# Performance work log

Measured on AMD Instinct MI355X. Metric: run time of the kernel, lower is better.

## Reference

```python
import jax, jax.numpy as jnp
import numpy as np

HIDDEN = 1024
HEADS = 16
HEAD = HIDDEN // HEADS
EXPAND = 4096
EPS = 1e-5


def layer_norm(x, g, b):
    mu = jnp.mean(x, axis=-1, keepdims=True)
    var = jnp.mean((x - mu) ** 2, axis=-1, keepdims=True)
    return (x - mu) * jax.lax.rsqrt(var + EPS) * g + b


def setup_inputs() -> dict:
    key = jax.random.key(0)
    ks = jax.random.split(key, 12)
    s = 0.02
    return {
        "x": jax.random.normal(ks[0], (4, 2048, HIDDEN), dtype=jnp.float32),
        "Wqkv": jax.random.normal(ks[1], (HIDDEN, 3 * HIDDEN), dtype=jnp.float32) * s,
        "bqkv": jnp.zeros((3 * HIDDEN,), jnp.float32),
        "Wproj": jax.random.normal(ks[2], (HIDDEN, HIDDEN), dtype=jnp.float32) * s,
        "bproj": jnp.zeros((HIDDEN,), jnp.float32),
        "W1": jax.random.normal(ks[3], (HIDDEN, EXPAND), dtype=jnp.float32) * s,
        "b1": jnp.zeros((EXPAND,), jnp.float32),
        "W2": jax.random.normal(ks[4], (EXPAND, HIDDEN), dtype=jnp.float32) * s,
        "b2": jnp.zeros((HIDDEN,), jnp.float32),
        "g1": jnp.ones((HIDDEN,), jnp.float32),
        "be1": jnp.zeros((HIDDEN,), jnp.float32),
        "g2": jnp.ones((HIDDEN,), jnp.float32),
        "be2": jnp.zeros((HIDDEN,), jnp.float32),
    }


def attention(x, Wqkv, bqkv, Wproj, bproj):
    B, L, _ = x.shape
    qkv = (x @ Wqkv + bqkv).reshape(B, L, 3, HEADS, HEAD)
    q, k, v = [qkv[:, :, i].transpose(0, 2, 1, 3) for i in range(3)]  # [B,H,L,D]
    attn = jnp.einsum("bnld,bnkd->bnlk", q, k) / np.sqrt(HEAD).astype(np.float32)
    attn = jax.nn.softmax(attn, axis=-1)
    o = jnp.einsum("bnlk,bnkd->bnld", attn, v)
    o = o.transpose(0, 2, 1, 3).reshape(B, L, HIDDEN)
    return o @ Wproj + bproj


def reference(x, Wqkv, bqkv, Wproj, bproj, W1, b1, W2, b2, g1, be1, g2, be2):
    # post-norm transformer block (pre_norm=False), dropout=0 (eval)
    h = layer_norm(x + attention(x, Wqkv, bqkv, Wproj, bproj), g1, be1)
    ff = jax.nn.gelu(h @ W1 + b1, approximate=False) @ W2 + b2
    return layer_norm(h + ff, g2, be2)
```

## Files before the change

### kernel.cpp

```cpp
#include <hip/hip_runtime.h>
#include <hip/hip_bf16.h>
#include <math.h>


typedef __bf16 bf16_t;
typedef __bf16 bf16x8 __attribute__((ext_vector_type(8)));
typedef __bf16 bf16x4 __attribute__((ext_vector_type(4)));
typedef float f32x4 __attribute__((ext_vector_type(4)));
typedef float f32x16 __attribute__((ext_vector_type(16)));

#define HID   1024
#define NHEAD 16
#define HD    64
#define EXPD  4096
#define LSEQ  2048
#define BATCH 4
#define MROWS (BATCH * LSEQ)

#if __has_builtin(__builtin_amdgcn_exp2f)
#define EXP2F __builtin_amdgcn_exp2f
#else
#define EXP2F exp2f
#endif

__device__ __forceinline__ void gld_lds16(const bf16_t* g, bf16_t* l) {
  __builtin_amdgcn_global_load_lds(
      (const __attribute__((address_space(1))) void*)g,
      (__attribute__((address_space(3))) void*)l, 16, 0, 0);
}

__device__ __forceinline__ void vmwait(int n) {
  if (n == 8)      asm volatile("s_waitcnt vmcnt(8)" ::: "memory");
  else if (n == 4) asm volatile("s_waitcnt vmcnt(4)" ::: "memory");
  else if (n == 3) asm volatile("s_waitcnt vmcnt(3)" ::: "memory");
  else if (n == 0) asm volatile("s_waitcnt vmcnt(0)" ::: "memory");
}

__device__ __forceinline__ void block_bar() {
  asm volatile("" ::: "memory");
  __builtin_amdgcn_s_barrier();
  asm volatile("" ::: "memory");
}

__device__ __forceinline__ void swap32(unsigned& a, unsigned& b) {
#if __has_builtin(__builtin_amdgcn_permlane32_swap)
  auto r = __builtin_amdgcn_permlane32_swap(a, b, false, false);
  a = r[0]; b = r[1];
#else
  bool hiL = ((threadIdx.x & 63) >= 32);
  unsigned pa = (unsigned)__shfl_xor((int)a, 32, 64);
  unsigned pb = (unsigned)__shfl_xor((int)b, 32, 64);
  unsigned na = hiL ? pb : a;
  unsigned nb = hiL ? b : pa;
  a = na; b = nb;
#endif
}

__device__ __forceinline__ unsigned pk_bf16(float lo, float hi) {
  bf16_t l = (bf16_t)lo, h = (bf16_t)hi;
  unsigned short ul, uh;
  __builtin_memcpy(&ul, &l, 2);
  __builtin_memcpy(&uh, &h, 2);
  return (unsigned)ul | ((unsigned)uh << 16);
}

__global__ __launch_bounds__(256) void cvt_bf16(const float* __restrict__ in,
                                                bf16_t* __restrict__ out, int n4) {
  int i = blockIdx.x * 256 + threadIdx.x;
  if (i >= n4) return;
  float4 v = ((const float4*)in)[i];
  bf16x4 o;
  o[0] = (bf16_t)v.x; o[1] = (bf16_t)v.y; o[2] = (bf16_t)v.z; o[3] = (bf16_t)v.w;
  ((bf16x4*)out)[i] = o;
}

__global__ __launch_bounds__(256) void transpose_cvt(const float* __restrict__ W,
                                                     bf16_t* __restrict__ Wt,
                                                     int K, int N) {
  __shared__ float tile[32][33];
  int n0 = blockIdx.x * 32, k0 = blockIdx.y * 32;
  int tx = threadIdx.x & 31, ty = threadIdx.x >> 5;
#pragma unroll
  for (int i = 0; i < 32; i += 8)
    tile[ty + i][tx] = W[(size_t)(k0 + ty + i) * N + n0 + tx];
  __syncthreads();
#pragma unroll
  for (int i = 0; i < 32; i += 8)
    Wt[(size_t)(n0 + ty + i) * K + k0 + tx] = (bf16_t)tile[tx][ty + i];
}

__global__ __launch_bounds__(256) void transpose_v(const bf16_t* __restrict__ qkvb,
                                                   bf16_t* __restrict__ vT) {
  __shared__ bf16_t tile[64][65];
  const int l0 = blockIdx.x * 64;
  const int bh = blockIdx.y;
  const int b = bh >> 4, h = bh & 15;
  const int tx = threadIdx.x & 63, ty = threadIdx.x >> 6;
  const bf16_t* src = qkvb + ((size_t)(b * LSEQ + l0)) * 3072 + 2048 + h * 64;
#pragma unroll
  for (int i = 0; i < 16; ++i) {
    int l = ty + 4 * i;
    tile[l][tx] = src[(size_t)l * 3072 + tx];
  }
  __syncthreads();
  bf16_t* dst = vT + ((size_t)bh * HD) * LSEQ + l0;
#pragma unroll
  for (int i = 0; i < 16; ++i) {
    int d = ty + 4 * i;
    dst[(size_t)d * LSEQ + tx] = tile[tx][d];
  }
}

template <int BM, int BN, int NTHR>
__global__ __launch_bounds__(NTHR, (NTHR == 512 ? 4 : 3))
void gemm_k(const bf16_t* __restrict__ A,
            const bf16_t* __restrict__ Bt,
            const float* __restrict__ bias,
            void* __restrict__ C,
            int M, int N, int K, int mode) {
  constexpr int WC = (NTHR / 64) / 2;
  constexpr int AL = BM * 4 / NTHR;
  constexpr int BL = BN * 4 / NTHR;
  constexpr int LOADS = AL + BL;
  constexpr int RSTEP = NTHR >> 2;
  __shared__ bf16_t As[3 * BM * 32];
  __shared__ bf16_t Bs[3 * BN * 32];

  const int nbx = gridDim.x;
  int p = blockIdx.y * nbx + blockIdx.x;
  const int GM = 8;
  int group = p / (GM * nbx);
  int idx = p - group * (GM * nbx);
  const int by = group * GM + (idx & (GM - 1));
  const int bx = idx >> 3;
  const int n0 = bx * BN, m0 = by * BM;

  const int t = threadIdx.x;
  const int lane = t & 63, w = t >> 6;
  const int wr = w / WC, wc = w % WC;
  const int quad = lane >> 4, l16 = lane & 15;

  f32x4 acc[4][4];
#pragma unroll
  for (int i = 0; i < 4; ++i)
#pragma unroll
    for (int j = 0; j < 4; ++j) acc[i][j] = (f32x4){0.f, 0.f, 0.f, 0.f};

  const int r0 = t >> 2;
  const unsigned ksw = (((unsigned)t & 3u) ^ ((unsigned)(r0 >> 1) & 3u)) * 8u;
  const unsigned offR0 = (unsigned)r0 * (unsigned)K + ksw;

  const bf16_t* aB = A + (size_t)m0 * K;
  const bf16_t* bB = Bt + (size_t)n0 * K;

  unsigned aoff[4], boff[4];
#pragma unroll
  for (int i = 0; i < 4; ++i) {
    int row = wr * 64 + 16 * i + l16;
    aoff[i] = (unsigned)(row * 32 + (quad ^ ((row >> 1) & 3)) * 8);
  }
#pragma unroll
  for (int j = 0; j < 4; ++j) {
    int row = wc * 64 + 16 * j + l16;
    boff[j] = (unsigned)(row * 32 + (quad ^ ((row >> 1) & 3)) * 8);
  }

  auto stage = [&](int slot, int kk) {
    bf16_t* Asl = As + slot * (BM * 32);
    bf16_t* Bsl = Bs + slot * (BN * 32);
    const bf16_t* aS = aB + kk;
    const bf16_t* bS = bB + kk;
#pragma unroll
    for (int a = 0; a < AL; ++a)
      gld_lds16(aS + offR0 + (size_t)a * RSTEP * K, Asl + (t + a * NTHR) * 8);
#pragma unroll
    for (int b = 0; b < BL; ++b)
      gld_lds16(bS + offR0 + (size_t)b * RSTEP * K, Bsl + (t + b * NTHR) * 8);
  };

  const int NT = K >> 5;

  stage(0, 0);
  stage(1, 32);
  vmwait(LOADS);
  block_bar();

  int cs = 0;
  for (int kt = 0; kt < NT; ++kt) {
    if (kt < NT - 2) {
      int ss = cs == 0 ? 2 : cs - 1;
      stage(ss, (kt + 2) * 32);
    }
    const bf16_t* Asl = As + cs * (BM * 32);
    const bf16_t* Bsl = Bs + cs * (BN * 32);
    bf16x8 af[4], bfr[4];
#pragma unroll
    for (int i = 0; i < 4; ++i) af[i] = *(const bf16x8*)(Asl + aoff[i]);
#pragma unroll
    for (int j = 0; j < 4; ++j) bfr[j] = *(const bf16x8*)(Bsl + boff[j]);
    __builtin_amdgcn_s_setprio(1);
#pragma unroll
    for (int i = 0; i < 4; ++i)
#pragma unroll
      for (int j = 0; j < 4; ++j)
        acc[i][j] = __builtin_amdgcn_mfma_f32_16x16x32_bf16(af[i], bfr[j], acc[i][j], 0, 0, 0);
    __builtin_amdgcn_s_setprio(0);
    if (kt < NT - 2)      vmwait(LOADS);
    else if (kt == NT - 2) vmwait(0);
    if (kt < NT - 1) block_bar();
    cs = cs == 2 ? 0 : cs + 1;
  }

#pragma unroll
  for (int i = 0; i < 4; ++i) {
    int rowb = m0 + wr * 64 + 16 * i + quad * 4;
#pragma unroll
    for (int j = 0; j < 4; ++j) {
      int col = n0 + wc * 64 + 16 * j + l16;
      float bv = bias[col];
#pragma unroll
      for (int r = 0; r < 4; ++r) {
        float v = acc[i][j][r] + bv;
        size_t idx = (size_t)(rowb + r) * N + col;
        if (mode == 0) {
          ((bf16_t*)C)[idx] = (bf16_t)v;
        } else if (mode == 1) {
          float u = v * (0.7978845608028654f + 0.0356774081f * v * v);
          float e = EXP2F(u * 2.885390082f);
          float th = (e - 1.f) / (e + 1.f);
          float gel = 0.5f * v * (1.f + th);
          ((bf16_t*)C)[idx] = (bf16_t)gel;
        } else {
          ((float*)C)[idx] = v;
        }
      }
    }
  }
}

__global__ __launch_bounds__(256, 2) void attn_kernel(const bf16_t* __restrict__ qkv,
                                                      const bf16_t* __restrict__ vT,
                                                      bf16_t* __restrict__ ob) {
  __shared__ bf16_t smem[5 * 128 * 64];
  bf16_t* Qs = smem + 32768;
  const int qt = blockIdx.x, h = blockIdx.y, b = blockIdx.z;
  const int t = threadIdx.x, lane = t & 63, w = t >> 6;
  const int l32 = lane & 31, hi = lane >> 5;
  const size_t RS = 3 * HID;
  const int bh = b * NHEAD + h;

  const bf16_t* qbase = qkv + ((size_t)(b * LSEQ + qt * 128)) * RS + h * HD;
  const bf16_t* kbase = qkv + ((size_t)b * LSEQ) * RS + HID + h * HD;
  const bf16_t* vtbase = vT + (size_t)bh * HD * LSEQ;

#pragma unroll
  for (int s = 0; s < 4; ++s) {
    int l = t + s * 256;
    int r = l >> 3, c8 = l & 7;
    gld_lds16(qbase + (size_t)r * RS + ((c8 ^ (r & 7)) * 8), Qs + l * 8);
  }
  __syncthreads();

  const float sc = 0.18033688011112042f;
  bf16x8 bq[4];
  {
    int qrow = 32 * w + l32;
#pragma unroll
    for (int c = 0; c < 4; ++c) {
      int y = 2 * c + hi;
      bf16x8 q8 = *(const bf16x8*)(Qs + qrow * 64 + ((y ^ (qrow & 7)) * 8));
#pragma unroll
      for (int e = 0; e < 8; ++e) q8[e] = (bf16_t)((float)q8[e] * sc);
      bq[c] = q8;
    }
  }

  auto stageKV = [&](int slot, int kt) {
    bf16_t* Ks = smem + slot * 16384;
    bf16_t* Vts = Ks + 8192;
#pragma unroll
    for (int s = 0; s < 4; ++s) {
      int l = t + s * 256;
      int r = l >> 3, c8 = l & 7;
      gld_lds16(kbase + (size_t)(kt * 128 + r) * RS + ((c8 ^ (r & 7)) * 8), Ks + l * 8);
      int rv = l >> 4, c16 = l & 15;
      gld_lds16(vtbase + (size_t)rv * LSEQ + kt * 128 + ((c16 ^ (rv & 7)) * 8), Vts + l * 8);
    }
  };

  f32x16 accO[2];
#pragma unroll
  for (int dt = 0; dt < 2; ++dt)
#pragma unroll
    for (int e = 0; e < 16; ++e) accO[dt][e] = 0.f;
  float l_acc = 0.f;

  constexpr int NT = LSEQ / 128;
  stageKV(0, 0);

  for (int kt = 0; kt < NT; ++kt) {
    const int cs = kt & 1;
    if (kt + 1 < NT) {
      stageKV(1 - cs, kt + 1);
      vmwait(8);
    } else {
      vmwait(0);
    }
    block_bar();
    const bf16_t* Ks = smem + cs * 16384;
    const bf16_t* Vts = Ks + 8192;

#pragma unroll
    for (int kt2 = 0; kt2 < 2; ++kt2) {
      f32x16 s0, s1;
#pragma unroll
      for (int e = 0; e < 16; ++e) { s0[e] = 0.f; s1[e] = 0.f; }
      __builtin_amdgcn_s_setprio(1);
#pragma unroll
      for (int c = 0; c < 4; ++c) {
        int y = 2 * c + hi;
        int r0 = (2 * kt2 + 0) * 32 + l32;
        bf16x8 a0 = *(const bf16x8*)(Ks + r0 * 64 + ((y ^ (r0 & 7)) * 8));
        s0 = __builtin_amdgcn_mfma_f32_32x32x16_bf16(a0, bq[c], s0, 0, 0, 0);
        int r1 = (2 * kt2 + 1) * 32 + l32;
        bf16x8 a1 = *(const bf16x8*)(Ks + r1 * 64 + ((y ^ (r1 & 7)) * 8));
        s1 = __builtin_amdgcn_mfma_f32_32x32x16_bf16(a1, bq[c], s1, 0, 0, 0);
      }
      __builtin_amdgcn_s_setprio(0);

      unsigned pf[2][2][4];
#pragma unroll
      for (int tile = 0; tile < 2; ++tile) {
        f32x16& sv = tile ? s1 : s0;
        float p[16];
#pragma unroll
        for (int e = 0; e < 16; ++e) { p[e] = EXP2F(sv[e]); l_acc += p[e]; }
        unsigned lo[4], hi_[4];
#pragma unroll
        for (int g = 0; g < 4; ++g) {
          lo[g] = pk_bf16(p[4 * g + 0], p[4 * g + 1]);
          hi_[g] = pk_bf16(p[4 * g + 2], p[4 * g + 3]);
        }
#pragma unroll
        for (int c2 = 0; c2 < 2; ++c2) {
          unsigned aL = lo[2 * c2], bL = lo[2 * c2 + 1];
          swap32(aL, bL);
          pf[tile][c2][0] = aL; pf[tile][c2][2] = bL;
          unsigned aH = hi_[2 * c2], bH = hi_[2 * c2 + 1];
          swap32(aH, bH);
          pf[tile][c2][1] = aH; pf[tile][c2][3] = bH;
        }
      }

      __builtin_amdgcn_s_setprio(1);
#pragma unroll
      for (int dt = 0; dt < 2; ++dt)
#pragma unroll
        for (int tile = 0; tile < 2; ++tile)
#pragma unroll
          for (int c2 = 0; c2 < 2; ++c2) {
            int ktile = 2 * kt2 + tile;
            int c8v = ktile * 4 + c2 * 2 + hi;
            int rv = dt * 32 + l32;
            bf16x8 av = *(const bf16x8*)(Vts + rv * 128 + ((c8v ^ (rv & 7)) * 8));
            union { unsigned u[4]; bf16x8 v; } bp;
            bp.u[0] = pf[tile][c2][0]; bp.u[1] = pf[tile][c2][1];
            bp.u[2] = pf[tile][c2][2]; bp.u[3] = pf[tile][c2][3];
            accO[dt] = __builtin_amdgcn_mfma_f32_32x32x16_bf16(av, bp.v, accO[dt], 0, 0, 0);
          }
      __builtin_amdgcn_s_setprio(0);
    }
    block_bar();
  }

  l_acc += __shfl_xor(l_acc, 32, 64);
  float inv = 1.f / l_acc;

  bf16_t* Osh = smem;
  {
    int q = 32 * w + l32;
#pragma unroll
    for (int dt = 0; dt < 2; ++dt)
#pragma unroll
      for (int e = 0; e < 16; ++e) {
        int d = dt * 32 + (e & 3) + 8 * (e >> 2) + 4 * hi;
        Osh[q * 68 + d] = (bf16_t)(accO[dt][e] * inv);
      }
  }
  __syncthreads();
#pragma unroll
  for (int s = 0; s < 4; ++s) {
    int l = t + s * 256;
    int r = l >> 3, c8 = l & 7;
    bf16x8 v = *(const bf16x8*)(Osh + r * 68 + c8 * 8);
    *(bf16x8*)(ob + ((size_t)(b * LSEQ + qt * 128 + r)) * HID + h * HD + c8 * 8) = v;
  }
}

__global__ __launch_bounds__(256) void resid_ln(const float* __restrict__ X,
                                                const float* __restrict__ Y,
                                                const float* __restrict__ g,
                                                const float* __restrict__ be,
                                                float* __restrict__ outf,
                                                bf16_t* __restrict__ outb) {
  const int row = blockIdx.x;
  const int t = threadIdx.x;
  float4 a = ((const float4*)X)[(size_t)row * 256 + t];
  float4 bvec = ((const float4*)Y)[(size_t)row * 256 + t];
  float v0 = a.x + bvec.x, v1 = a.y + bvec.y, v2 = a.z + bvec.z, v3 = a.w + bvec.w;
  float s = v0 + v1 + v2 + v3;
  float s2 = v0 * v0 + v1 * v1 + v2 * v2 + v3 * v3;
#pragma unroll
  for (int msk = 1; msk < 64; msk <<= 1) {
    s += __shfl_xor(s, msk, 64);
    s2 += __shfl_xor(s2, msk, 64);
  }
  __shared__ float red[8];
  int w = t >> 6;
  if ((t & 63) == 0) { red[w] = s; red[w + 4] = s2; }
  __syncthreads();
  s = red[0] + red[1] + red[2] + red[3];
  s2 = red[4] + red[5] + red[6] + red[7];
  float mu = s * (1.f / 1024.f);
  float var = s2 * (1.f / 1024.f) - mu * mu;
  float rstd = rsqrtf(var + 1e-5f);
  float4 gg = ((const float4*)g)[t];
  float4 bb = ((const float4*)be)[t];
  float o0 = (v0 - mu) * rstd * gg.x + bb.x;
  float o1 = (v1 - mu) * rstd * gg.y + bb.y;
  float o2 = (v2 - mu) * rstd * gg.z + bb.z;
  float o3 = (v3 - mu) * rstd * gg.w + bb.w;
  float4 o = {o0, o1, o2, o3};
  ((float4*)outf)[(size_t)row * 256 + t] = o;
  if (outb) {
    bf16x4 ob4;
    ob4[0] = (bf16_t)o0; ob4[1] = (bf16_t)o1; ob4[2] = (bf16_t)o2; ob4[3] = (bf16_t)o3;
    ((bf16x4*)outb)[(size_t)row * 256 + t] = ob4;
  }
}

extern "C" void kernel_launch(void* const* d_in, const int* in_sizes, int n_in,
                              void* d_out, int out_size, void* d_ws, size_t ws_size,
                              hipStream_t stream) {
  const float* x     = (const float*)d_in[0];
  const float* Wqkv  = (const float*)d_in[1];
  const float* bqkv  = (const float*)d_in[2];
  const float* Wproj = (const float*)d_in[3];
  const float* bproj = (const float*)d_in[4];
  const float* W1    = (const float*)d_in[5];
  const float* b1    = (const float*)d_in[6];
  const float* W2    = (const float*)d_in[7];
  const float* b2    = (const float*)d_in[8];
  const float* g1    = (const float*)d_in[9];
  const float* be1   = (const float*)d_in[10];
  const float* g2    = (const float*)d_in[11];
  const float* be2   = (const float*)d_in[12];
  float* out = (float*)d_out;

  char* ws = (char*)d_ws;
  size_t off = 0;
  auto alloc = [&](size_t bytes) -> char* {
    char* p = ws + off;
    off += (bytes + 255) & ~(size_t)255;
    return p;
  };
  bf16_t* wqkvT  = (bf16_t*)alloc((size_t)3072 * 1024 * 2);
  bf16_t* wprojT = (bf16_t*)alloc((size_t)1024 * 1024 * 2);
  bf16_t* w1T    = (bf16_t*)alloc((size_t)4096 * 1024 * 2);
  bf16_t* w2T    = (bf16_t*)alloc((size_t)1024 * 4096 * 2);
  char*   xb_ob  = alloc((size_t)MROWS * HID * 2);
  char*   qkv_ff = alloc((size_t)MROWS * EXPD * 2);
  char*   a_f2   = alloc((size_t)MROWS * HID * 4);
  float*  h      = (float*)alloc((size_t)MROWS * HID * 4);
  bf16_t* hb     = (bf16_t*)alloc((size_t)MROWS * HID * 2);

  bf16_t* xb    = (bf16_t*)xb_ob;
  bf16_t* ob    = (bf16_t*)xb_ob;
  bf16_t* qkvb  = (bf16_t*)qkv_ff;
  bf16_t* ff1b  = (bf16_t*)qkv_ff;
  float*  attnf = (float*)a_f2;
  float*  ff2f  = (float*)a_f2;
  bf16_t* vTg   = hb;

  dim3 blk(256);
  dim3 blk512(512);
  transpose_cvt<<<dim3(3072 / 32, 1024 / 32), blk, 0, stream>>>(Wqkv, wqkvT, 1024, 3072);
  transpose_cvt<<<dim3(1024 / 32, 1024 / 32), blk, 0, stream>>>(Wproj, wprojT, 1024, 1024);
  transpose_cvt<<<dim3(4096 / 32, 1024 / 32), blk, 0, stream>>>(W1, w1T, 1024, 4096);
  transpose_cvt<<<dim3(1024 / 32, 4096 / 32), blk, 0, stream>>>(W2, w2T, 4096, 1024);
  cvt_bf16<<<MROWS * HID / 4 / 256, blk, 0, stream>>>(x, xb, MROWS * HID / 4);

  gemm_k<128, 256, 512><<<dim3(3072 / 256, MROWS / 128), blk512, 0, stream>>>(
      xb, wqkvT, bqkv, qkvb, MROWS, 3072, 1024, 0);
  transpose_v<<<dim3(LSEQ / 64, BATCH * NHEAD), blk, 0, stream>>>(qkvb, vTg);
  attn_kernel<<<dim3(LSEQ / 128, NHEAD, BATCH), blk, 0, stream>>>(qkvb, vTg, ob);
  gemm_k<128, 128, 256><<<dim3(1024 / 128, MROWS / 128), blk, 0, stream>>>(
      ob, wprojT, bproj, attnf, MROWS, 1024, 1024, 2);
  resid_ln<<<MROWS, blk, 0, stream>>>(x, attnf, g1, be1, h, hb);
  gemm_k<128, 256, 512><<<dim3(4096 / 256, MROWS / 128), blk512, 0, stream>>>(
      hb, w1T, b1, ff1b, MROWS, 4096, 1024, 1);
  gemm_k<128, 128, 256><<<dim3(1024 / 128, MROWS / 128), blk, 0, stream>>>(
      ff1b, w2T, b2, ff2f, MROWS, 1024, 4096, 2);
  resid_ln<<<MROWS, blk, 0, stream>>>(h, ff2f, g2, be2, out, (bf16_t*)nullptr);
}
```

Before: 569.1 us.

## Split-K the FFN down-projection GEMM and fold partial sums into LayerNorm

Adds split-K support to the GEMM kernel through blockIdx.z. The second FFN GEMM now runs with 128x256 tiles, 512 threads and two K halves, and the second half writes its partial sum to a separate fp32 buffer. The final residual LayerNorm reads and adds that extra partial, so no separate reduction kernel is needed. The workspace is laid out manually so the partial buffer reuses the dead weight and activation regions. The goal is to put more workgroups on the long-K GEMM, at the cost of an extra 32MB fp32 write and read.

After: 550.5 us. 1.03x faster.

```diff
diff --git a/kernel.cpp b/kernel.cpp
--- a/kernel.cpp
+++ b/kernel.cpp
@@ -117,6 +117,7 @@
             const bf16_t* __restrict__ Bt,
             const float* __restrict__ bias,
             void* __restrict__ C,
+            float* __restrict__ C2,
             int M, int N, int K, int mode) {
   constexpr int WC = (NTHR / 64) / 2;
   constexpr int AL = BM * 4 / NTHR;
@@ -135,6 +136,10 @@
   const int bx = idx >> 3;
   const int n0 = bx * BN, m0 = by * BM;
 
+  const int zz = blockIdx.z;
+  const int kLen = K / (int)gridDim.z;
+  const int kOff = zz * kLen;
+
   const int t = threadIdx.x;
   const int lane = t & 63, w = t >> 6;
   const int wr = w / WC, wc = w % WC;
@@ -150,8 +155,8 @@
   const unsigned ksw = (((unsigned)t & 3u) ^ ((unsigned)(r0 >> 1) & 3u)) * 8u;
   const unsigned offR0 = (unsigned)r0 * (unsigned)K + ksw;
 
-  const bf16_t* aB = A + (size_t)m0 * K;
-  const bf16_t* bB = Bt + (size_t)n0 * K;
+  const bf16_t* aB = A + (size_t)m0 * K + kOff;
+  const bf16_t* bB = Bt + (size_t)n0 * K + kOff;
 
   unsigned aoff[4], boff[4];
 #pragma unroll
@@ -178,7 +183,7 @@
       gld_lds16(bS + offR0 + (size_t)b * RSTEP * K, Bsl + (t + b * NTHR) * 8);
   };
 
-  const int NT = K >> 5;
+  const int NT = kLen >> 5;
 
   stage(0, 0);
   stage(1, 32);
@@ -217,12 +222,14 @@
 #pragma unroll
     for (int j = 0; j < 4; ++j) {
       int col = n0 + wc * 64 + 16 * j + l16;
-      float bv = bias[col];
+      float bv = (zz == 0) ? bias[col] : 0.f;
 #pragma unroll
       for (int r = 0; r < 4; ++r) {
         float v = acc[i][j][r] + bv;
         size_t idx = (size_t)(rowb + r) * N + col;
-        if (mode == 0) {
+        if (zz != 0) {
+          C2[idx] = v;
+        } else if (mode == 0) {
           ((bf16_t*)C)[idx] = (bf16_t)v;
         } else if (mode == 1) {
           float u = v * (0.7978845608028654f + 0.0356774081f * v * v);
@@ -399,6 +406,7 @@
 
 __global__ __launch_bounds__(256) void resid_ln(const float* __restrict__ X,
                                                 const float* __restrict__ Y,
+                                                const float* __restrict__ Y2,
                                                 const float* __restrict__ g,
                                                 const float* __restrict__ be,
                                                 float* __restrict__ outf,
@@ -407,7 +415,10 @@
   const int t = threadIdx.x;
   float4 a = ((const float4*)X)[(size_t)row * 256 + t];
   float4 bvec = ((const float4*)Y)[(size_t)row * 256 + t];
-  float v0 = a.x + bvec.x, v1 = a.y + bvec.y, v2 = a.z + bvec.z, v3 = a.w + bvec.w;
+  float4 cvec = {0.f, 0.f, 0.f, 0.f};
+  if (Y2) cvec = ((const float4*)Y2)[(size_t)row * 256 + t];
+  float v0 = a.x + bvec.x + cvec.x, v1 = a.y + bvec.y + cvec.y;
+  float v2 = a.z + bvec.z + cvec.z, v3 = a.w + bvec.w + cvec.w;
   float s = v0 + v1 + v2 + v3;
   float s2 = v0 * v0 + v1 * v1 + v2 * v2 + v3 * v3;
 #pragma unroll
@@ -458,28 +469,24 @@
   float* out = (float*)d_out;
 
   char* ws = (char*)d_ws;
-  size_t off = 0;
-  auto alloc = [&](size_t bytes) -> char* {
-    char* p = ws + off;
-    off += (bytes + 255) & ~(size_t)255;
-    return p;
-  };
-  bf16_t* wqkvT  = (bf16_t*)alloc((size_t)3072 * 1024 * 2);
-  bf16_t* wprojT = (bf16_t*)alloc((size_t)1024 * 1024 * 2);
-  bf16_t* w1T    = (bf16_t*)alloc((size_t)4096 * 1024 * 2);
-  bf16_t* w2T    = (bf16_t*)alloc((size_t)1024 * 4096 * 2);
-  char*   xb_ob  = alloc((size_t)MROWS * HID * 2);
-  char*   qkv_ff = alloc((size_t)MROWS * EXPD * 2);
-  char*   a_f2   = alloc((size_t)MROWS * HID * 4);
-  float*  h      = (float*)alloc((size_t)MROWS * HID * 4);
-  bf16_t* hb     = (bf16_t*)alloc((size_t)MROWS * HID * 2);
+  bf16_t* w2T    = (bf16_t*)(ws);
+  float*  h      = (float*) (ws + ((size_t)8 << 20));
+  float*  a_f2   = (float*) (ws + ((size_t)40 << 20));
+  bf16_t* qkv_ff = (bf16_t*)(ws + ((size_t)72 << 20));
+  char*   E      = ws + ((size_t)136 << 20);
+  bf16_t* wqkvT  = (bf16_t*)(E);
+  bf16_t* wprojT = (bf16_t*)(E + ((size_t)6 << 20));
+  bf16_t* w1T    = (bf16_t*)(E + ((size_t)8 << 20));
+  char*   xb_ob  = E + ((size_t)16 << 20);
+  bf16_t* hb     = (bf16_t*)(E + ((size_t)32 << 20));
+  float*  f2b    = (float*)E;
 
   bf16_t* xb    = (bf16_t*)xb_ob;
   bf16_t* ob    = (bf16_t*)xb_ob;
-  bf16_t* qkvb  = (bf16_t*)qkv_ff;
-  bf16_t* ff1b  = (bf16_t*)qkv_ff;
-  float*  attnf = (float*)a_f2;
-  float*  ff2f  = (float*)a_f2;
+  bf16_t* qkvb  = qkv_ff;
+  bf16_t* ff1b  = qkv_ff;
+  float*  attnf = a_f2;
+  float*  ff2f  = a_f2;
   bf16_t* vTg   = hb;
 
   dim3 blk(256);
@@ -491,15 +498,15 @@
   cvt_bf16<<<MROWS * HID / 4 / 256, blk, 0, stream>>>(x, xb, MROWS * HID / 4);
 
   gemm_k<128, 256, 512><<<dim3(3072 / 256, MROWS / 128), blk512, 0, stream>>>(
-      xb, wqkvT, bqkv, qkvb, MROWS, 3072, 1024, 0);
+      xb, wqkvT, bqkv, qkvb, nullptr, MROWS, 3072, 1024, 0);
   transpose_v<<<dim3(LSEQ / 64, BATCH * NHEAD), blk, 0, stream>>>(qkvb, vTg);
   attn_kernel<<<dim3(LSEQ / 128, NHEAD, BATCH), blk, 0, stream>>>(qkvb, vTg, ob);
   gemm_k<128, 128, 256><<<dim3(1024 / 128, MROWS / 128), blk, 0, stream>>>(
-      ob, wprojT, bproj, attnf, MROWS, 1024, 1024, 2);
-  resid_ln<<<MROWS, blk, 0, stream>>>(x, attnf, g1, be1, h, hb);
+      ob, wprojT, bproj, attnf, nullptr, MROWS, 1024, 1024, 2);
+  resid_ln<<<MROWS, blk, 0, stream>>>(x, attnf, nullptr, g1, be1, h, hb);
   gemm_k<128, 256, 512><<<dim3(4096 / 256, MROWS / 128), blk512, 0, stream>>>(
-      hb, w1T, b1, ff1b, MROWS, 4096, 1024, 1);
-  gemm_k<128, 128, 256><<<dim3(1024 / 128, MROWS / 128), blk, 0, stream>>>(
-      ff1b, w2T, b2, ff2f, MROWS, 1024, 4096, 2);
-  resid_ln<<<MROWS, blk, 0, stream>>>(h, ff2f, g2, be2, out, (bf16_t*)nullptr);
-}
+      hb, w1T, b1, ff1b, nullptr, MROWS, 4096, 1024, 1);
+  gemm_k<128, 256, 512><<<dim3(1024 / 256, MROWS / 128, 2), blk512, 0, stream>>>(
+      ff1b, w2T, b2, ff2f, f2b, MROWS, 1024, 4096, 2);
+  resid_ln<<<MROWS, blk, 0, stream>>>(h, ff2f, f2b, g2, be2, out, (bf16_t*)nullptr);
+}
```
